# Kernel tuning notes

Measured on AMD Instinct MI355X. Metric: run time of the kernel, lower is better.

Reference implementation:

```python
import jax, jax.numpy as jnp
import numpy as np

PAD = 1  # deform_conv2d called with stride=1, padding=1, dilation=1 in forward


def _bilinear_gather(x, py, px):
    """Bilinear sample x [B,C,H,W] at float coords py,px [B,K,Ho,Wo].
    Out-of-bounds corners contribute zero (torchvision deform_conv2d semantics).
    Returns [B,C,K,Ho,Wo]."""
    B, C, H, W = x.shape
    y0 = jnp.floor(py)
    x0 = jnp.floor(px)
    y1, x1 = y0 + 1.0, x0 + 1.0
    wy1 = py - y0
    wy0 = 1.0 - wy1
    wx1 = px - x0
    wx0 = 1.0 - wx1
    x_flat = x.reshape(B, C, H * W)

    def corner(yi, xi, w):
        m = ((yi >= 0) & (yi < H) & (xi >= 0) & (xi < W)).astype(x.dtype)
        yc = jnp.clip(yi, 0, H - 1).astype(jnp.int32)
        xc = jnp.clip(xi, 0, W - 1).astype(jnp.int32)
        lin = (yc * W + xc).reshape(B, -1)  # [B, K*Ho*Wo]
        vals = jax.vmap(lambda xf, idx: jnp.take(xf, idx, axis=1))(x_flat, lin)
        vals = vals.reshape(B, C, *yi.shape[1:])  # [B,C,K,Ho,Wo]
        return vals * (w * m)[:, None]

    return (corner(y0, x0, wy0 * wx0) + corner(y0, x1, wy0 * wx1)
            + corner(y1, x0, wy1 * wx0) + corner(y1, x1, wy1 * wx1))


def reference(x, w_off, b_off, weight):
    B, C, H, W = x.shape
    O, Ci, kh, kw = weight.shape
    K = kh * kw
    # offset conv: Conv2d(C -> 2*k*k, kernel 3, stride 1, pad 1, groups=1)
    offset = jax.lax.conv_general_dilated(
        x, w_off, window_strides=(1, 1), padding=[(PAD, PAD), (PAD, PAD)],
        dimension_numbers=('NCHW', 'OIHW', 'NCHW')) + b_off[None, :, None, None]
    off = offset.reshape(B, K, 2, H, W)  # channel layout: (tap, [dy, dx])

    ky = jnp.repeat(jnp.arange(kh, dtype=x.dtype), kw)  # [K] kernel row index
    kx = jnp.tile(jnp.arange(kw, dtype=x.dtype), kh)    # [K] kernel col index
    ys = jnp.arange(H, dtype=x.dtype)[None, None, :, None]  # [1,1,H,1]
    xs = jnp.arange(W, dtype=x.dtype)[None, None, None, :]  # [1,1,1,W]
    py = ys + (ky - PAD)[None, :, None, None] + off[:, :, 0]  # [B,K,H,W]
    px = xs + (kx - PAD)[None, :, None, None] + off[:, :, 1]

    sampled = _bilinear_gather(x, py, px)  # [B,C,K,H,W]
    out = jnp.einsum('bckhw,ock->bohw', sampled, weight.reshape(O, Ci, K))
    return out


def setup_inputs() -> dict:
    key = jax.random.key(0)
    k1, k2, k3 = jax.random.split(key, 3)
    x = jax.random.normal(k1, (4, 64, 128, 128), dtype=jnp.float32)
    # small offset-conv weights -> modest learned offsets (realistic DCN behavior)
    w_off = jax.random.normal(k2, (18, 64, 3, 3), dtype=jnp.float32) * 0.01
    b_off = jnp.zeros((18,), dtype=jnp.float32)
    weight = jax.random.normal(k3, (64, 64, 3, 3), dtype=jnp.float32)
    return {'x': x, 'w_off': w_off, 'b_off': b_off, 'weight': weight}
```

## Files before the change

### kernel.cpp

```cpp
#include <hip/hip_runtime.h>
#include <math.h>

typedef _Float16 f16;
typedef _Float16 f16x8 __attribute__((ext_vector_type(8)));
typedef float f32x4 __attribute__((ext_vector_type(4)));

namespace {
constexpr int Bn = 4;
constexpr int Cn = 64;
constexpr int On = 64;
constexpr int Hn = 128;
constexpr int Wn = 128;
constexpr int Kn = 9;
constexpr int HWn = Hn * Wn;
constexpr int CKn = Cn * Kn;
constexpr int NPIX = Bn * HWn;
constexpr int SR = 72;
}

__global__ __launch_bounds__(256) void prep_weights(
    const float* __restrict__ w_off, const float* __restrict__ weight,
    f16* __restrict__ wofb, f16* __restrict__ wtb) {
  int t = blockIdx.x * 256 + threadIdx.x;
  if (t < Kn * On * Cn) {
    int c = t & 63, o = (t >> 6) & 63, k = t >> 12;
    wtb[t] = (f16)weight[((o << 6) + c) * 9 + k];
  }
  if (t < Kn * 32 * Cn) {
    int c = t & 63, o = (t >> 6) & 31, k = t >> 11;
    float v = (o < 18) ? w_off[((o << 6) + c) * 9 + k] : 0.f;
    wofb[t] = (f16)v;
  }
}

__global__ __launch_bounds__(256) void transpose_x(
    const float* __restrict__ x, f16* __restrict__ xt) {
  const int l = threadIdx.x & 63;
  const int cw = threadIdx.x >> 6;
  const int pixbase = blockIdx.x * 64;
  const int b = pixbase >> 14;
  const int hw = (pixbase & (HWn - 1)) + l;

  f16x8 v0, v1;
#pragma unroll
  for (int i = 0; i < 8; ++i) {
    v0[i] = (f16)x[((size_t)(b * Cn + cw * 16 + i)) * HWn + hw];
    v1[i] = (f16)x[((size_t)(b * Cn + cw * 16 + 8 + i)) * HWn + hw];
  }
  f16* dst = xt + ((size_t)(b * HWn + hw)) * 64 + cw * 16;
  *(f16x8*)dst = v0;
  *(f16x8*)(dst + 8) = v1;
}

__global__ __launch_bounds__(256, 4) void dcn_fused(
    const f16* __restrict__ xt, const f16* __restrict__ wofb,
    const f16* __restrict__ wtb, const float* __restrict__ b_off,
    float* __restrict__ out) {
  __shared__ __align__(16) f16 Sb[3][64 * SR];
  __shared__ float off_lds[64][20];

  const int t = threadIdx.x;
  const int px_s = t >> 2, cq = t & 3;
  const int pixbase = blockIdx.x * 64;
  const int b = pixbase >> 14;
  const int y = (pixbase & (HWn - 1)) >> 7;
  const int xx0 = pixbase & (Wn - 1);
  const int xx = xx0 + px_s;
  const f16* xb = xt + ((size_t)b * HWn) * 64;

  const int lane = t & 63, wv = t >> 6;
  const int l15 = lane & 15, q = lane >> 4;

  {
    const int mA = wv & 1;
    const int nbA = (wv >> 1) * 2;
    f32x4 accA[2];
#pragma unroll
    for (int t2 = 0; t2 < 2; ++t2) accA[t2] = (f32x4){0.f, 0.f, 0.f, 0.f};

    for (int g = 0; g < 3; ++g) {
      if (g) __syncthreads();

      f16x8 wfA[3][2];
#pragma unroll
      for (int j = 0; j < 3; ++j)
#pragma unroll
        for (int s = 0; s < 2; ++s)
          wfA[j][s] = *(const f16x8*)(wofb +
              (((size_t)((3 * g + j) * 32 + mA * 16 + l15)) << 6) +
              s * 32 + q * 8);

#pragma unroll
      for (int j = 0; j < 3; ++j) {
        const int k = 3 * g + j;
        const int dy = k / 3 - 1, dx = k % 3 - 1;
        const int ys = y + dy, xs = xx + dx;
        f16* sdst = &Sb[j][px_s * SR + cq * 16];
        if (ys >= 0 && ys < Hn && xs >= 0 && xs < Wn) {
          const f16* src = xb + (size_t)(ys * Wn + xs) * 64 + cq * 16;
          *(f16x8*)sdst = *(const f16x8*)src;
          *(f16x8*)(sdst + 8) = *(const f16x8*)(src + 8);
        } else {
          f16x8 z = {};
          *(f16x8*)sdst = z;
          *(f16x8*)(sdst + 8) = z;
        }
      }
      __syncthreads();

#pragma unroll
      for (int j = 0; j < 3; ++j)
#pragma unroll
        for (int s = 0; s < 2; ++s)
#pragma unroll
          for (int t2 = 0; t2 < 2; ++t2) {
            f16x8 bf = *(const f16x8*)
                &Sb[j][((nbA + t2) * 16 + l15) * SR + s * 32 + q * 8];
            accA[t2] = __builtin_amdgcn_mfma_f32_16x16x32_f16(wfA[j][s], bf,
                                                              accA[t2],
                                                              0, 0, 0);
          }
    }

#pragma unroll
    for (int t2 = 0; t2 < 2; ++t2)
#pragma unroll
      for (int r = 0; r < 4; ++r) {
        int o = mA * 16 + q * 4 + r;
        if (o < 18) {
          int pxl = (nbA + t2) * 16 + l15;
          off_lds[pxl][o] = accA[t2][r] + b_off[o];
        }
      }
    __syncthreads();
  }

  const int obase = wv * 16;
  float2 off9[9];
#pragma unroll
  for (int k = 0; k < Kn; ++k)
    off9[k] = *(const float2*)&off_lds[px_s][2 * k];

  f32x4 acc[4];
#pragma unroll
  for (int pt = 0; pt < 4; ++pt) acc[pt] = (f32x4){0.f, 0.f, 0.f, 0.f};

  for (int g = 0; g < 3; ++g) {
    if (g) __syncthreads();

    f16x8 wf[3][2];
#pragma unroll
    for (int j = 0; j < 3; ++j)
#pragma unroll
      for (int s = 0; s < 2; ++s)
        wf[j][s] = *(const f16x8*)(wtb +
            (((size_t)((3 * g + j) * 64 + obase + l15)) << 6) + s * 32 + q * 8);

#pragma unroll
    for (int j = 0; j < 3; ++j) {
      const int k = 3 * g + j;
      const int dy = k / 3 - 1, dx = k % 3 - 1;
      float py = (float)(y + dy) + off9[k].x;
      float pxf = (float)(xx + dx) + off9[k].y;
      float y0f = floorf(py), x0f = floorf(pxf);
      int y0 = (int)y0f, x0 = (int)x0f;
      int y1 = y0 + 1, x1 = x0 + 1;
      float wy1 = py - y0f, wx1 = pxf - x0f;
      float wy0 = 1.f - wy1, wx0 = 1.f - wx1;
      float my0 = (y0 >= 0 && y0 < Hn) ? 1.f : 0.f;
      float my1 = (y1 >= 0 && y1 < Hn) ? 1.f : 0.f;
      float mx0 = (x0 >= 0 && x0 < Wn) ? 1.f : 0.f;
      float mx1 = (x1 >= 0 && x1 < Wn) ? 1.f : 0.f;
      f16 h00 = (f16)(wy0 * wx0 * my0 * mx0);
      f16 h01 = (f16)(wy0 * wx1 * my0 * mx1);
      f16 h10 = (f16)(wy1 * wx0 * my1 * mx0);
      f16 h11 = (f16)(wy1 * wx1 * my1 * mx1);
      int cy0 = min(max(y0, 0), Hn - 1), cy1 = min(max(y1, 0), Hn - 1);
      int cx0 = min(max(x0, 0), Wn - 1), cx1 = min(max(x1, 0), Wn - 1);
      const f16* r00 = xb + (size_t)(cy0 * Wn + cx0) * 64 + cq * 16;
      const f16* r01 = xb + (size_t)(cy0 * Wn + cx1) * 64 + cq * 16;
      const f16* r10 = xb + (size_t)(cy1 * Wn + cx0) * 64 + cq * 16;
      const f16* r11 = xb + (size_t)(cy1 * Wn + cx1) * 64 + cq * 16;
      f16* sdst = &Sb[j][px_s * SR + cq * 16];
#pragma unroll
      for (int h = 0; h < 2; ++h) {
        f16x8 a = *(const f16x8*)(r00 + h * 8);
        f16x8 b2 = *(const f16x8*)(r01 + h * 8);
        f16x8 c = *(const f16x8*)(r10 + h * 8);
        f16x8 d = *(const f16x8*)(r11 + h * 8);
        f16x8 v = a * h00 + b2 * h01 + c * h10 + d * h11;
        *(f16x8*)(sdst + h * 8) = v;
      }
    }
    __syncthreads();

#pragma unroll
    for (int j = 0; j < 3; ++j)
#pragma unroll
      for (int s = 0; s < 2; ++s)
#pragma unroll
        for (int pt = 0; pt < 4; ++pt) {
          f16x8 bf =
              *(const f16x8*)&Sb[j][(pt * 16 + l15) * SR + s * 32 + q * 8];
          acc[pt] = __builtin_amdgcn_mfma_f32_16x16x32_f16(wf[j][s], bf,
                                                           acc[pt], 0, 0, 0);
        }
  }

  float* ob = out + (size_t)b * On * HWn + (y * Wn + xx0);
#pragma unroll
  for (int pt = 0; pt < 4; ++pt) {
#pragma unroll
    for (int r = 0; r < 4; ++r) {
      int o = obase + q * 4 + r;
      ob[(size_t)o * HWn + pt * 16 + l15] = acc[pt][r];
    }
  }
}

extern "C" void kernel_launch(void* const* d_in, const int* in_sizes, int n_in,
                              void* d_out, int out_size, void* d_ws, size_t ws_size,
                              hipStream_t stream) {
  const float* x = (const float*)d_in[0];
  const float* w_off = (const float*)d_in[1];
  const float* b_off = (const float*)d_in[2];
  const float* weight = (const float*)d_in[3];
  float* out = (float*)d_out;

  f16* xt = (f16*)d_ws;
  f16* wtb = xt + (size_t)NPIX * Cn;
  f16* wofb = wtb + Kn * On * Cn;

  prep_weights<<<dim3(144), dim3(256), 0, stream>>>(w_off, weight, wofb, wtb);
  transpose_x<<<dim3(NPIX / 64), dim3(256), 0, stream>>>(x, xt);
  dcn_fused<<<dim3(NPIX / 64), dim3(256), 0, stream>>>(xt, wofb, wtb, b_off,
                                                       out);
}
```

Baseline: 113.4 us.

## Shrink DCN tile to 32 pixels with 2-wave blocks and fuse weight prep into transpose

The main kernel now processes 32 pixels per block with 128 threads. Each wave computes 32 output channels over 2 pixel tiles, where before it computed 16 channels over 4 tiles. This doubles the grid size and halves LDS per block, aiming for more concurrent blocks and better latency hiding on the gather-heavy bilinear path. The separate weight-prep launch is folded into the transpose kernel, which removes one launch. In exchange, each block reloads the full offset and main weights over a smaller pixel tile, so weight traffic per pixel goes up.

```diff
diff --git a/kernel.cpp b/kernel.cpp
--- a/kernel.cpp
+++ b/kernel.cpp
@@ -13,28 +13,14 @@
 constexpr int Wn = 128;
 constexpr int Kn = 9;
 constexpr int HWn = Hn * Wn;
-constexpr int CKn = Cn * Kn;
 constexpr int NPIX = Bn * HWn;
 constexpr int SR = 72;
 }
 
-__global__ __launch_bounds__(256) void prep_weights(
-    const float* __restrict__ w_off, const float* __restrict__ weight,
+__global__ __launch_bounds__(256) void transpose_prep(
+    const float* __restrict__ x, const float* __restrict__ w_off,
+    const float* __restrict__ weight, f16* __restrict__ xt,
     f16* __restrict__ wofb, f16* __restrict__ wtb) {
-  int t = blockIdx.x * 256 + threadIdx.x;
-  if (t < Kn * On * Cn) {
-    int c = t & 63, o = (t >> 6) & 63, k = t >> 12;
-    wtb[t] = (f16)weight[((o << 6) + c) * 9 + k];
-  }
-  if (t < Kn * 32 * Cn) {
-    int c = t & 63, o = (t >> 6) & 31, k = t >> 11;
-    float v = (o < 18) ? w_off[((o << 6) + c) * 9 + k] : 0.f;
-    wofb[t] = (f16)v;
-  }
-}
-
-__global__ __launch_bounds__(256) void transpose_x(
-    const float* __restrict__ x, f16* __restrict__ xt) {
   const int l = threadIdx.x & 63;
   const int cw = threadIdx.x >> 6;
   const int pixbase = blockIdx.x * 64;
@@ -50,18 +36,31 @@
   f16* dst = xt + ((size_t)(b * HWn + hw)) * 64 + cw * 16;
   *(f16x8*)dst = v0;
   *(f16x8*)(dst + 8) = v1;
-}
-
-__global__ __launch_bounds__(256, 4) void dcn_fused(
+
+  if (blockIdx.x < 144) {
+    int t = blockIdx.x * 256 + threadIdx.x;
+    {
+      int c = t & 63, o = (t >> 6) & 63, k = t >> 12;
+      wtb[t] = (f16)weight[((o << 6) + c) * 9 + k];
+    }
+    if (t < Kn * 32 * Cn) {
+      int c = t & 63, o = (t >> 6) & 31, k = t >> 11;
+      float v = (o < 18) ? w_off[((o << 6) + c) * 9 + k] : 0.f;
+      wofb[t] = (f16)v;
+    }
+  }
+}
+
+__global__ __launch_bounds__(128, 4) void dcn_fused(
     const f16* __restrict__ xt, const f16* __restrict__ wofb,
     const f16* __restrict__ wtb, const float* __restrict__ b_off,
     float* __restrict__ out) {
-  __shared__ __align__(16) f16 Sb[3][64 * SR];
-  __shared__ float off_lds[64][20];
+  __shared__ __align__(16) f16 Sb[3][32 * SR];
+  __shared__ float off_lds[32][20];
 
   const int t = threadIdx.x;
   const int px_s = t >> 2, cq = t & 3;
-  const int pixbase = blockIdx.x * 64;
+  const int pixbase = blockIdx.x * 32;
   const int b = pixbase >> 14;
   const int y = (pixbase & (HWn - 1)) >> 7;
   const int xx0 = pixbase & (Wn - 1);
@@ -72,11 +71,9 @@
   const int l15 = lane & 15, q = lane >> 4;
 
   {
-    const int mA = wv & 1;
-    const int nbA = (wv >> 1) * 2;
     f32x4 accA[2];
 #pragma unroll
-    for (int t2 = 0; t2 < 2; ++t2) accA[t2] = (f32x4){0.f, 0.f, 0.f, 0.f};
+    for (int pt = 0; pt < 2; ++pt) accA[pt] = (f32x4){0.f, 0.f, 0.f, 0.f};
 
     for (int g = 0; g < 3; ++g) {
       if (g) __syncthreads();
@@ -87,7 +84,7 @@
 #pragma unroll
         for (int s = 0; s < 2; ++s)
           wfA[j][s] = *(const f16x8*)(wofb +
-              (((size_t)((3 * g + j) * 32 + mA * 16 + l15)) << 6) +
+              (((size_t)((3 * g + j) * 32 + wv * 16 + l15)) << 6) +
               s * 32 + q * 8);
 
 #pragma unroll
@@ -113,48 +110,52 @@
 #pragma unroll
         for (int s = 0; s < 2; ++s)
 #pragma unroll
-          for (int t2 = 0; t2 < 2; ++t2) {
+          for (int pt = 0; pt < 2; ++pt) {
             f16x8 bf = *(const f16x8*)
-                &Sb[j][((nbA + t2) * 16 + l15) * SR + s * 32 + q * 8];
-            accA[t2] = __builtin_amdgcn_mfma_f32_16x16x32_f16(wfA[j][s], bf,
-                                                              accA[t2],
+                &Sb[j][(pt * 16 + l15) * SR + s * 32 + q * 8];
+            accA[pt] = __builtin_amdgcn_mfma_f32_16x16x32_f16(wfA[j][s], bf,
+                                                              accA[pt],
                                                               0, 0, 0);
           }
     }
 
 #pragma unroll
-    for (int t2 = 0; t2 < 2; ++t2)
+    for (int pt = 0; pt < 2; ++pt)
 #pragma unroll
       for (int r = 0; r < 4; ++r) {
-        int o = mA * 16 + q * 4 + r;
+        int o = wv * 16 + q * 4 + r;
         if (o < 18) {
-          int pxl = (nbA + t2) * 16 + l15;
-          off_lds[pxl][o] = accA[t2][r] + b_off[o];
+          int pxl = pt * 16 + l15;
+          off_lds[pxl][o] = accA[pt][r] + b_off[o];
         }
       }
     __syncthreads();
   }
 
-  const int obase = wv * 16;
   float2 off9[9];
 #pragma unroll
   for (int k = 0; k < Kn; ++k)
     off9[k] = *(const float2*)&off_lds[px_s][2 * k];
 
-  f32x4 acc[4];
-#pragma unroll
-  for (int pt = 0; pt < 4; ++pt) acc[pt] = (f32x4){0.f, 0.f, 0.f, 0.f};
+  f32x4 acc[2][2];
+#pragma unroll
+  for (int ot = 0; ot < 2; ++ot)
+#pragma unroll
+    for (int pt = 0; pt < 2; ++pt) acc[ot][pt] = (f32x4){0.f, 0.f, 0.f, 0.f};
 
   for (int g = 0; g < 3; ++g) {
     if (g) __syncthreads();
 
-    f16x8 wf[3][2];
+    f16x8 wf[3][2][2];
 #pragma unroll
     for (int j = 0; j < 3; ++j)
 #pragma unroll
-      for (int s = 0; s < 2; ++s)
-        wf[j][s] = *(const f16x8*)(wtb +
-            (((size_t)((3 * g + j) * 64 + obase + l15)) << 6) + s * 32 + q * 8);
+      for (int ot = 0; ot < 2; ++ot)
+#pragma unroll
+        for (int s = 0; s < 2; ++s)
+          wf[j][ot][s] = *(const f16x8*)(wtb +
+              (((size_t)((3 * g + j) * 64 + wv * 32 + ot * 16 + l15)) << 6) +
+              s * 32 + q * 8);
 
 #pragma unroll
     for (int j = 0; j < 3; ++j) {
@@ -199,23 +200,26 @@
 #pragma unroll
       for (int s = 0; s < 2; ++s)
 #pragma unroll
-        for (int pt = 0; pt < 4; ++pt) {
+        for (int pt = 0; pt < 2; ++pt) {
           f16x8 bf =
               *(const f16x8*)&Sb[j][(pt * 16 + l15) * SR + s * 32 + q * 8];
-          acc[pt] = __builtin_amdgcn_mfma_f32_16x16x32_f16(wf[j][s], bf,
-                                                           acc[pt], 0, 0, 0);
+#pragma unroll
+          for (int ot = 0; ot < 2; ++ot)
+            acc[ot][pt] = __builtin_amdgcn_mfma_f32_16x16x32_f16(
+                wf[j][ot][s], bf, acc[ot][pt], 0, 0, 0);
         }
   }
 
   float* ob = out + (size_t)b * On * HWn + (y * Wn + xx0);
 #pragma unroll
-  for (int pt = 0; pt < 4; ++pt) {
-#pragma unroll
-    for (int r = 0; r < 4; ++r) {
-      int o = obase + q * 4 + r;
-      ob[(size_t)o * HWn + pt * 16 + l15] = acc[pt][r];
-    }
-  }
+  for (int ot = 0; ot < 2; ++ot)
+#pragma unroll
+    for (int pt = 0; pt < 2; ++pt)
+#pragma unroll
+      for (int r = 0; r < 4; ++r) {
+        int o = wv * 32 + ot * 16 + q * 4 + r;
+        ob[(size_t)o * HWn + pt * 16 + l15] = acc[ot][pt][r];
+      }
 }
 
 extern "C" void kernel_launch(void* const* d_in, const int* in_sizes, int n_in,
@@ -231,8 +235,8 @@
   f16* wtb = xt + (size_t)NPIX * Cn;
   f16* wofb = wtb + Kn * On * Cn;
 
-  prep_weights<<<dim3(144), dim3(256), 0, stream>>>(w_off, weight, wofb, wtb);
-  transpose_x<<<dim3(NPIX / 64), dim3(256), 0, stream>>>(x, xt);
-  dcn_fused<<<dim3(NPIX / 64), dim3(256), 0, stream>>>(xt, wofb, wtb, b_off,
+  transpose_prep<<<dim3(NPIX / 64), dim3(256), 0, stream>>>(x, w_off, weight,
+                                                            xt, wofb, wtb);
+  dcn_fused<<<dim3(NPIX / 32), dim3(128), 0, stream>>>(xt, wofb, wtb, b_off,
                                                        out);
 }
```

After: 114.3 us. Within noise of the previous version (+0.8%).
